# Kernel optimization log

Hardware: AMD Instinct MI355X
Metric: run time of the kernel (lower is better)

The kernel has to match this reference:

```python
import jax, jax.numpy as jnp
import numpy as np

GROUPS = 32
EPS = 1e-6


def group_norm(x, gamma, beta):
    b, c, h, w = x.shape
    xg = x.reshape(b, GROUPS, c // GROUPS, h, w)
    mu = xg.mean(axis=(2, 3, 4), keepdims=True)
    var = xg.var(axis=(2, 3, 4), keepdims=True)
    xn = ((xg - mu) * jax.lax.rsqrt(var + EPS)).reshape(b, c, h, w)
    return xn * gamma[None, :, None, None] + beta[None, :, None, None]


def conv1x1(x, w, b):
    # x: (b,c_in,h,w), w: (c_out,c_in), b: (c_out,)
    return jnp.einsum('oc,bchw->bohw', w, x) + b[None, :, None, None]


def setup_inputs() -> dict:
    key = jax.random.key(0)
    ks = jax.random.split(key, 10)
    c = 512
    scale = 1.0 / np.sqrt(c)
    inp = jax.random.normal(ks[0], (16, c, 32, 32), dtype=jnp.float32)
    return {
        'inp': inp,
        'gamma': jnp.ones((c,), jnp.float32),
        'beta': jnp.zeros((c,), jnp.float32),
        'Wq': jax.random.normal(ks[1], (c, c), jnp.float32) * scale,
        'bq': jnp.zeros((c,), jnp.float32),
        'Wk': jax.random.normal(ks[2], (c, c), jnp.float32) * scale,
        'bk': jnp.zeros((c,), jnp.float32),
        'Wv': jax.random.normal(ks[3], (c, c), jnp.float32) * scale,
        'bv': jnp.zeros((c,), jnp.float32),
        'Wo': jax.random.normal(ks[4], (c, c), jnp.float32) * scale,
        'bo': jnp.zeros((c,), jnp.float32),
    }


def reference(inp, gamma, beta, Wq, bq, Wk, bk, Wv, bv, Wo, bo):
    b, c, h, w = inp.shape
    x = group_norm(inp, gamma, beta)
    Q = conv1x1(x, Wq, bq).reshape(b, c, h * w)  # (b,c,n)
    K = conv1x1(x, Wk, bk).reshape(b, c, h * w)  # (b,c,m)
    V = conv1x1(x, Wv, bv).reshape(b, c, h * w)  # (b,c,m)
    # attn[b,n,m] = sum_c Q[b,c,n] * K[b,c,m], scaled then softmax over m
    attn = jnp.einsum('bcn,bcm->bnm', Q, K) / jnp.sqrt(jnp.float32(c))
    attn = jax.nn.softmax(attn, axis=2)
    # A[b,c,n] = sum_m V[b,c,m] * attn[b,n,m]  (== bmm(V, attn^T))
    A = jnp.einsum('bcm,bnm->bcn', V, attn).reshape(b, c, h, w)
    A = conv1x1(A, Wo, bo)
    return inp + A
```

## Files before the change

### kernel.cpp

```cpp
#include <hip/hip_runtime.h>

typedef unsigned short UST;
typedef __attribute__((ext_vector_type(8))) short bf16x8;
typedef __attribute__((ext_vector_type(8))) unsigned short us8;
typedef __attribute__((ext_vector_type(4))) float f32x4;

__device__ __forceinline__ UST f2bf(float f) {
  union { float f; unsigned int u; } x; x.f = f;
  unsigned int r = x.u + 0x7fffu + ((x.u >> 16) & 1u);
  return (UST)(r >> 16);
}
__device__ __forceinline__ float bf2f(UST h) {
  union { unsigned int u; float f; } x; x.u = ((unsigned int)h) << 16;
  return x.f;
}

__device__ __forceinline__ void sync_lds() {
  asm volatile("s_waitcnt lgkmcnt(0)\n\ts_barrier" ::: "memory");
}
__device__ __forceinline__ void barrier_nowait() {
  asm volatile("s_barrier" ::: "memory");
}

__global__ __launch_bounds__(256) void conv_w(
    const float4* __restrict__ wq, const float4* __restrict__ wk,
    const float4* __restrict__ wv, const float4* __restrict__ wo,
    ushort4* __restrict__ oqkv, ushort4* __restrict__ owo,
    const float4* __restrict__ bq4, const float4* __restrict__ bk4,
    const float4* __restrict__ bv4, float4* __restrict__ bqkv4) {
  int i = blockIdx.x * 256 + threadIdx.x;
  float4 v;
  v = wq[i]; oqkv[i]          = make_ushort4(f2bf(v.x), f2bf(v.y), f2bf(v.z), f2bf(v.w));
  v = wk[i]; oqkv[i + 65536]  = make_ushort4(f2bf(v.x), f2bf(v.y), f2bf(v.z), f2bf(v.w));
  v = wv[i]; oqkv[i + 131072] = make_ushort4(f2bf(v.x), f2bf(v.y), f2bf(v.z), f2bf(v.w));
  v = wo[i]; owo[i]           = make_ushort4(f2bf(v.x), f2bf(v.y), f2bf(v.z), f2bf(v.w));
  if (blockIdx.x < 2) {
    int t = blockIdx.x * 256 + threadIdx.x;
    if (t < 384) bqkv4[t] = (t < 128) ? bq4[t] : (t < 256 ? bk4[t - 128] : bv4[t - 256]);
  }
}

__global__ __launch_bounds__(256) void gn_fused(
    const float* __restrict__ inp, const float* __restrict__ gamma,
    const float* __restrict__ beta, UST* __restrict__ Xnt) {
  const int g = blockIdx.x & 31, b = blockIdx.x >> 5;
  const int tid = threadIdx.x;
  const float* base = inp + ((size_t)b * 32 + g) * 16384;
  const float4* p4 = (const float4*)base;
  float s = 0.f, ss = 0.f;
#pragma unroll
  for (int i = 0; i < 16; i++) {
    float4 t = p4[tid + i * 256];
    s += t.x + t.y + t.z + t.w;
    ss += t.x * t.x + t.y * t.y + t.z * t.z + t.w * t.w;
  }
  for (int o = 32; o >= 1; o >>= 1) { s += __shfl_xor(s, o); ss += __shfl_xor(ss, o); }
  __shared__ float red[8];
  __shared__ float mu_s, rstd_s;
  const int w = tid >> 6;
  if ((tid & 63) == 0) { red[w * 2] = s; red[w * 2 + 1] = ss; }
  __syncthreads();
  if (tid == 0) {
    float S1 = red[0] + red[2] + red[4] + red[6];
    float S2 = red[1] + red[3] + red[5] + red[7];
    float mu = S1 * (1.f / 16384.f);
    float var = S2 * (1.f / 16384.f) - mu * mu;
    mu_s = mu; rstd_s = rsqrtf(var + 1e-6f);
  }
  __syncthreads();
  const float mu = mu_s, rstd = rstd_s;
#pragma unroll
  for (int cc = 0; cc < 2; cc++) {
    const int ccg = g * 2 + cc;
    float sc[8], sh[8];
#pragma unroll
    for (int j = 0; j < 8; j++) {
      int ch = ccg * 8 + j;
      sc[j] = gamma[ch] * rstd;
      sh[j] = beta[ch] - mu * sc[j];
    }
#pragma unroll
    for (int i = 0; i < 4; i++) {
      const int n = tid + i * 256;
      us8 v;
#pragma unroll
      for (int j = 0; j < 8; j++) {
        float x = inp[((size_t)b * 512 + ccg * 8 + j) * 1024 + n];
        v[j] = f2bf(x * sc[j] + sh[j]);
      }
      *(us8*)(Xnt + (size_t)b * 524288 + (size_t)ccg * 8192 + (size_t)n * 8) = v;
    }
  }
}

__global__ __launch_bounds__(256) void softmax_k(const UST* __restrict__ S,
                                                 UST* __restrict__ P) {
  const int w = threadIdx.x >> 6, lane = threadIdx.x & 63;
  const size_t row = (size_t)blockIdx.x * 4 + w;
  const us8* Sr = (const us8*)(S + row * 1024);
  us8 a = Sr[lane], b = Sr[64 + lane];
  float v[16];
#pragma unroll
  for (int j = 0; j < 8; j++) { v[j] = bf2f(a[j]); v[8 + j] = bf2f(b[j]); }
  float m = v[0];
#pragma unroll
  for (int i = 1; i < 16; i++) m = fmaxf(m, v[i]);
#pragma unroll
  for (int o = 32; o >= 1; o >>= 1) m = fmaxf(m, __shfl_xor(m, o));
  float s = 0.f;
#pragma unroll
  for (int i = 0; i < 16; i++) { v[i] = __expf(v[i] - m); s += v[i]; }
#pragma unroll
  for (int o = 32; o >= 1; o >>= 1) s += __shfl_xor(s, o);
  const float rs = 1.f / s;
  us8* Pr = (us8*)(P + row * 1024);
  us8 oa, ob;
#pragma unroll
  for (int j = 0; j < 8; j++) { oa[j] = f2bf(v[j] * rs); ob[j] = f2bf(v[8 + j] * rs); }
  Pr[lane] = oa; Pr[64 + lane] = ob;
}

template <int EPI>
__global__ __launch_bounds__(256, 2) void gemm_bt(
    const UST* __restrict__ A, const UST* __restrict__ B, void* __restrict__ C,
    const float* __restrict__ bias, const float* __restrict__ extra, float scale,
    int K, int ldc,
    int rsA, int csA, int ssA, int rsB, int csB, int ssB,
    long zA, long zB, long zC) {
  __shared__ __align__(16) UST buf[10240];
  UST* lA = buf;
  UST* lB = buf + 5120;

  const int tid = threadIdx.x;
  const int z = blockIdx.z;
  const int m0 = blockIdx.y * 128;
  const int n0 = blockIdx.x * 128;
  const UST* Ab = A + (long)z * zA;
  const UST* Bb = B + (long)z * zB;

  const int w = tid >> 6, lane = tid & 63;
  const int quad = lane >> 4, l16 = lane & 15;
  const int wm = w >> 1, wn = w & 1;

  f32x4 acc[4][4];
#pragma unroll
  for (int i = 0; i < 4; i++)
#pragma unroll
    for (int j = 0; j < 4; j++) acc[i][j] = f32x4{0.f, 0.f, 0.f, 0.f};

  const int rowa = tid >> 2;
  const int kchunk = tid & 3;
  const UST* gA = Ab + (size_t)(m0 + rowa) * rsA + (size_t)kchunk * csA;
  const UST* gB = Bb + (size_t)(n0 + rowa) * rsB + (size_t)kchunk * csB;
  const size_t a64 = (size_t)64 * rsA, b64 = (size_t)64 * rsB;
  UST* wA = lA + rowa * 40 + kchunk * 8;
  UST* wB = lB + rowa * 40 + kchunk * 8;

  us8 pa0 = *(const us8*)gA, pa1 = *(const us8*)(gA + a64);
  us8 pb0 = *(const us8*)gB, pb1 = *(const us8*)(gB + b64);

  const int nk = K >> 5;
  for (int k = 0; k < nk; ++k) {
    us8 na0, na1, nb0, nb1;
    if (k + 1 < nk) {
      gA += ssA; gB += ssB;
      na0 = *(const us8*)gA; na1 = *(const us8*)(gA + a64);
      nb0 = *(const us8*)gB; nb1 = *(const us8*)(gB + b64);
    }
    if (k) barrier_nowait();
    *(us8*)wA = pa0; *(us8*)(wA + 2560) = pa1;
    *(us8*)wB = pb0; *(us8*)(wB + 2560) = pb1;
    sync_lds();
    bf16x8 af[4], bfr[4];
#pragma unroll
    for (int i = 0; i < 4; i++)
      af[i] = *(const bf16x8*)(lA + (wm * 64 + i * 16 + l16) * 40 + quad * 8);
#pragma unroll
    for (int j = 0; j < 4; j++)
      bfr[j] = *(const bf16x8*)(lB + (wn * 64 + j * 16 + l16) * 40 + quad * 8);
#pragma unroll
    for (int i = 0; i < 4; i++)
#pragma unroll
      for (int j = 0; j < 4; j++)
        acc[i][j] = __builtin_amdgcn_mfma_f32_16x16x32_bf16(af[i], bfr[j], acc[i][j], 0, 0, 0);
    pa0 = na0; pa1 = na1; pb0 = nb0; pb1 = nb1;
  }

  barrier_nowait();

  if constexpr (EPI == 4) {
    float* fbuf = (float*)buf;
    float* Cb = (float*)C + (long)z * zC;
    const float* Eb = extra + (long)z * zC;
#pragma unroll
    for (int p = 0; p < 4; ++p) {
      if (p) barrier_nowait();
      if (wm == (p >> 1)) {
#pragma unroll
        for (int ii = 0; ii < 2; ii++) {
          const int i = (p & 1) * 2 + ii;
#pragma unroll
          for (int j = 0; j < 4; j++)
#pragma unroll
            for (int r = 0; r < 4; r++)
              fbuf[(ii * 16 + quad * 4 + r) * 132 + wn * 64 + j * 16 + l16] = acc[i][j][r];
        }
      }
      sync_lds();
#pragma unroll
      for (int it = 0; it < 4; ++it) {
        int q = tid + it * 256;
        int row = q >> 5, colc = q & 31;
        int gr = m0 + p * 32 + row;
        size_t off = (size_t)gr * ldc + n0 + colc * 4;
        float4 v = *(float4*)&fbuf[row * 132 + colc * 4];
        float4 e = *(const float4*)&Eb[off];
        float bb = bias[gr];
        v.x += bb + e.x; v.y += bb + e.y; v.z += bb + e.z; v.w += bb + e.w;
        *(float4*)&Cb[off] = v;
      }
    }
  } else {
    const bool vreg = (EPI == 6) && (n0 >= 1024);
    if (!vreg) {
      UST* Cb = (UST*)C + (long)z * zC;
#pragma unroll
      for (int h = 0; h < 2; ++h) {
        if (h) barrier_nowait();
        if (wm == h) {
#pragma unroll
          for (int i = 0; i < 4; i++)
#pragma unroll
            for (int j = 0; j < 4; j++) {
              float bc = 0.f;
              if constexpr (EPI == 6) bc = bias[n0 + wn * 64 + j * 16 + l16];
#pragma unroll
              for (int r = 0; r < 4; r++) {
                float v = acc[i][j][r] + bc;
                if constexpr (EPI == 5) v *= scale;
                buf[(i * 16 + quad * 4 + r) * 136 + wn * 64 + j * 16 + l16] = f2bf(v);
              }
            }
        }
        sync_lds();
#pragma unroll
        for (int it = 0; it < 4; ++it) {
          int q = tid + it * 256;
          int row = q >> 4, colc = q & 15;
          us8 v = *(us8*)&buf[row * 136 + colc * 8];
          *(us8*)&Cb[(size_t)(m0 + h * 64 + row) * ldc + n0 + colc * 8] = v;
        }
      }
    } else {
      UST* Vb = (UST*)extra + (long)z * 524288;
#pragma unroll
      for (int h = 0; h < 2; ++h) {
        if (h) barrier_nowait();
        if (wn == h) {
#pragma unroll
          for (int i = 0; i < 4; i++)
#pragma unroll
            for (int j = 0; j < 4; j++) {
              const float bc = bias[n0 + wn * 64 + j * 16 + l16];
#pragma unroll
              for (int r = 0; r < 4; r++) {
                float v = acc[i][j][r] + bc;
                buf[(j * 16 + l16) * 136 + wm * 64 + i * 16 + quad * 4 + r] = f2bf(v);
              }
            }
        }
        sync_lds();
#pragma unroll
        for (int it = 0; it < 4; ++it) {
          int q = tid + it * 256;
          int c = q >> 4, mc = q & 15;
          us8 v = *(us8*)&buf[c * 136 + mc * 8];
          *(us8*)&Vb[(size_t)(n0 - 1024 + h * 64 + c) * 1024 + m0 + mc * 8] = v;
        }
      }
    }
  }
}

extern "C" void kernel_launch(void* const* d_in, const int* in_sizes, int n_in,
                              void* d_out, int out_size, void* d_ws, size_t ws_size,
                              hipStream_t stream) {
  const float* inp   = (const float*)d_in[0];
  const float* gamma = (const float*)d_in[1];
  const float* beta  = (const float*)d_in[2];
  const float* Wq    = (const float*)d_in[3];
  const float* bq    = (const float*)d_in[4];
  const float* Wk    = (const float*)d_in[5];
  const float* bk    = (const float*)d_in[6];
  const float* Wv    = (const float*)d_in[7];
  const float* bv    = (const float*)d_in[8];
  const float* Wo    = (const float*)d_in[9];
  const float* bo    = (const float*)d_in[10];
  float* out = (float*)d_out;
  char* ws = (char*)d_ws;

  UST*   Xnt   = (UST*)(ws);
  UST*   QKt   = (UST*)(ws + ((size_t)16 << 20));
  UST*   V     = (UST*)(ws + ((size_t)48 << 20));
  UST*   S     = (UST*)(ws + ((size_t)64 << 20));
  float* bqkv  = (float*)(ws + ((size_t)96 << 20));
  UST*   Wqkvb = (UST*)(ws + ((size_t)96 << 20) + 8192);
  UST*   Wob   = Wqkvb + 786432;
  UST*   P     = QKt;
  UST*   At    = Xnt;

  conv_w<<<256, 256, 0, stream>>>(
      (const float4*)Wq, (const float4*)Wk, (const float4*)Wv, (const float4*)Wo,
      (ushort4*)Wqkvb, (ushort4*)Wob,
      (const float4*)bq, (const float4*)bk, (const float4*)bv, (float4*)bqkv);
  gn_fused<<<512, 256, 0, stream>>>(inp, gamma, beta, Xnt);

  gemm_bt<6><<<dim3(12, 8, 16), 256, 0, stream>>>(
      Xnt, Wqkvb, QKt, bqkv, (const float*)V, 1.f,
      512, 1024, 8, 8192, 32768, 512, 8, 32, 524288, 0, 1048576);
  gemm_bt<5><<<dim3(8, 8, 16), 256, 0, stream>>>(
      QKt, QKt + 512, S, nullptr, nullptr, 0.04419417382415922f,
      512, 1024, 1024, 8, 32, 1024, 8, 32, 1048576, 1048576, 1048576);
  softmax_k<<<4096, 256, 0, stream>>>(S, P);
  gemm_bt<3><<<dim3(4, 8, 16), 256, 0, stream>>>(
      P, V, At, nullptr, nullptr, 1.f,
      1024, 512, 1024, 8, 32, 1024, 8, 32, 1048576, 524288, 524288);
  gemm_bt<4><<<dim3(8, 4, 16), 256, 0, stream>>>(
      Wob, At, out, bo, inp, 1.f,
      512, 1024, 512, 8, 32, 512, 8, 32, 0, 524288, 524288);
}
```

Before: 238.5 us.

## Double-buffer GEMM LDS tiles, merge prep kernels, swizzle QKV block order

```diff
diff --git a/kernel.cpp b/kernel.cpp
--- a/kernel.cpp
+++ b/kernel.cpp
@@ -22,29 +22,30 @@
   asm volatile("s_barrier" ::: "memory");
 }
 
-__global__ __launch_bounds__(256) void conv_w(
+__global__ __launch_bounds__(256) void prep(
+    const float* __restrict__ inp, const float* __restrict__ gamma,
+    const float* __restrict__ beta, UST* __restrict__ Xnt,
     const float4* __restrict__ wq, const float4* __restrict__ wk,
     const float4* __restrict__ wv, const float4* __restrict__ wo,
     ushort4* __restrict__ oqkv, ushort4* __restrict__ owo,
     const float4* __restrict__ bq4, const float4* __restrict__ bk4,
     const float4* __restrict__ bv4, float4* __restrict__ bqkv4) {
-  int i = blockIdx.x * 256 + threadIdx.x;
-  float4 v;
-  v = wq[i]; oqkv[i]          = make_ushort4(f2bf(v.x), f2bf(v.y), f2bf(v.z), f2bf(v.w));
-  v = wk[i]; oqkv[i + 65536]  = make_ushort4(f2bf(v.x), f2bf(v.y), f2bf(v.z), f2bf(v.w));
-  v = wv[i]; oqkv[i + 131072] = make_ushort4(f2bf(v.x), f2bf(v.y), f2bf(v.z), f2bf(v.w));
-  v = wo[i]; owo[i]           = make_ushort4(f2bf(v.x), f2bf(v.y), f2bf(v.z), f2bf(v.w));
-  if (blockIdx.x < 2) {
-    int t = blockIdx.x * 256 + threadIdx.x;
-    if (t < 384) bqkv4[t] = (t < 128) ? bq4[t] : (t < 256 ? bk4[t - 128] : bv4[t - 256]);
-  }
-}
-
-__global__ __launch_bounds__(256) void gn_fused(
-    const float* __restrict__ inp, const float* __restrict__ gamma,
-    const float* __restrict__ beta, UST* __restrict__ Xnt) {
+  const int tid = threadIdx.x;
+  if (blockIdx.x >= 512) {
+    const int wb = blockIdx.x - 512;
+    int i = wb * 256 + tid;
+    float4 v;
+    v = wq[i]; oqkv[i]          = make_ushort4(f2bf(v.x), f2bf(v.y), f2bf(v.z), f2bf(v.w));
+    v = wk[i]; oqkv[i + 65536]  = make_ushort4(f2bf(v.x), f2bf(v.y), f2bf(v.z), f2bf(v.w));
+    v = wv[i]; oqkv[i + 131072] = make_ushort4(f2bf(v.x), f2bf(v.y), f2bf(v.z), f2bf(v.w));
+    v = wo[i]; owo[i]           = make_ushort4(f2bf(v.x), f2bf(v.y), f2bf(v.z), f2bf(v.w));
+    if (wb < 2) {
+      int t = wb * 256 + tid;
+      if (t < 384) bqkv4[t] = (t < 128) ? bq4[t] : (t < 256 ? bk4[t - 128] : bv4[t - 256]);
+    }
+    return;
+  }
   const int g = blockIdx.x & 31, b = blockIdx.x >> 5;
-  const int tid = threadIdx.x;
   const float* base = inp + ((size_t)b * 32 + g) * 16384;
   const float4* p4 = (const float4*)base;
   float s = 0.f, ss = 0.f;
@@ -120,21 +121,30 @@
   Pr[lane] = oa; Pr[64 + lane] = ob;
 }
 
-template <int EPI>
+template <int EPI, bool SWZ>
 __global__ __launch_bounds__(256, 2) void gemm_bt(
     const UST* __restrict__ A, const UST* __restrict__ B, void* __restrict__ C,
     const float* __restrict__ bias, const float* __restrict__ extra, float scale,
     int K, int ldc,
     int rsA, int csA, int ssA, int rsB, int csB, int ssB,
     long zA, long zB, long zC) {
-  __shared__ __align__(16) UST buf[10240];
-  UST* lA = buf;
-  UST* lB = buf + 5120;
+  __shared__ __align__(16) UST buf[20480];
+  UST* l0A = buf;
+  UST* l0B = buf + 5120;
+  UST* l1A = buf + 10240;
+  UST* l1B = buf + 15360;
 
   const int tid = threadIdx.x;
-  const int z = blockIdx.z;
-  const int m0 = blockIdx.y * 128;
-  const int n0 = blockIdx.x * 128;
+  int m0, n0, z;
+  if constexpr (SWZ) {
+    int lin = blockIdx.x + 12 * (blockIdx.y + 8 * blockIdx.z);
+    int g = lin & 7, idx = lin >> 3;
+    int al = idx / 12, x = idx - al * 12;
+    int at = g * 16 + al;
+    m0 = (at & 7) * 128; n0 = x * 128; z = at >> 3;
+  } else {
+    m0 = blockIdx.y * 128; n0 = blockIdx.x * 128; z = blockIdx.z;
+  }
   const UST* Ab = A + (long)z * zA;
   const UST* Bb = B + (long)z * zB;
 
@@ -153,40 +163,51 @@
   const UST* gA = Ab + (size_t)(m0 + rowa) * rsA + (size_t)kchunk * csA;
   const UST* gB = Bb + (size_t)(n0 + rowa) * rsB + (size_t)kchunk * csB;
   const size_t a64 = (size_t)64 * rsA, b64 = (size_t)64 * rsB;
-  UST* wA = lA + rowa * 40 + kchunk * 8;
-  UST* wB = lB + rowa * 40 + kchunk * 8;
+  const int lw = rowa * 40 + kchunk * 8;
+
+  const int nk = K >> 5;
 
   us8 pa0 = *(const us8*)gA, pa1 = *(const us8*)(gA + a64);
   us8 pb0 = *(const us8*)gB, pb1 = *(const us8*)(gB + b64);
-
-  const int nk = K >> 5;
+  *(us8*)(l0A + lw) = pa0; *(us8*)(l0A + lw + 2560) = pa1;
+  *(us8*)(l0B + lw) = pb0; *(us8*)(l0B + lw + 2560) = pb1;
+  if (nk > 1) {
+    gA += ssA; gB += ssB;
+    pa0 = *(const us8*)gA; pa1 = *(const us8*)(gA + a64);
+    pb0 = *(const us8*)gB; pb1 = *(const us8*)(gB + b64);
+  }
+  sync_lds();
+
   for (int k = 0; k < nk; ++k) {
-    us8 na0, na1, nb0, nb1;
+    UST* curA = (k & 1) ? l1A : l0A;
+    UST* curB = (k & 1) ? l1B : l0B;
+    UST* nxtA = (k & 1) ? l0A : l1A;
+    UST* nxtB = (k & 1) ? l0B : l1B;
     if (k + 1 < nk) {
+      *(us8*)(nxtA + lw) = pa0; *(us8*)(nxtA + lw + 2560) = pa1;
+      *(us8*)(nxtB + lw) = pb0; *(us8*)(nxtB + lw + 2560) = pb1;
+    }
+    us8 qa0, qa1, qb0, qb1;
+    if (k + 2 < nk) {
       gA += ssA; gB += ssB;
-      na0 = *(const us8*)gA; na1 = *(const us8*)(gA + a64);
-      nb0 = *(const us8*)gB; nb1 = *(const us8*)(gB + b64);
-    }
-    if (k) barrier_nowait();
-    *(us8*)wA = pa0; *(us8*)(wA + 2560) = pa1;
-    *(us8*)wB = pb0; *(us8*)(wB + 2560) = pb1;
-    sync_lds();
+      qa0 = *(const us8*)gA; qa1 = *(const us8*)(gA + a64);
+      qb0 = *(const us8*)gB; qb1 = *(const us8*)(gB + b64);
+    }
     bf16x8 af[4], bfr[4];
 #pragma unroll
     for (int i = 0; i < 4; i++)
-      af[i] = *(const bf16x8*)(lA + (wm * 64 + i * 16 + l16) * 40 + quad * 8);
+      af[i] = *(const bf16x8*)(curA + (wm * 64 + i * 16 + l16) * 40 + quad * 8);
 #pragma unroll
     for (int j = 0; j < 4; j++)
-      bfr[j] = *(const bf16x8*)(lB + (wn * 64 + j * 16 + l16) * 40 + quad * 8);
+      bfr[j] = *(const bf16x8*)(curB + (wn * 64 + j * 16 + l16) * 40 + quad * 8);
 #pragma unroll
     for (int i = 0; i < 4; i++)
 #pragma unroll
       for (int j = 0; j < 4; j++)
         acc[i][j] = __builtin_amdgcn_mfma_f32_16x16x32_bf16(af[i], bfr[j], acc[i][j], 0, 0, 0);
-    pa0 = na0; pa1 = na1; pb0 = nb0; pb1 = nb1;
-  }
-
-  barrier_nowait();
+    sync_lds();
+    pa0 = qa0; pa1 = qa1; pb0 = qb0; pb1 = qb1;
+  }
 
   if constexpr (EPI == 4) {
     float* fbuf = (float*)buf;
@@ -309,23 +330,23 @@
   UST*   P     = QKt;
   UST*   At    = Xnt;
 
-  conv_w<<<256, 256, 0, stream>>>(
+  prep<<<768, 256, 0, stream>>>(
+      inp, gamma, beta, Xnt,
       (const float4*)Wq, (const float4*)Wk, (const float4*)Wv, (const float4*)Wo,
       (ushort4*)Wqkvb, (ushort4*)Wob,
       (const float4*)bq, (const float4*)bk, (const float4*)bv, (float4*)bqkv);
-  gn_fused<<<512, 256, 0, stream>>>(inp, gamma, beta, Xnt);
-
-  gemm_bt<6><<<dim3(12, 8, 16), 256, 0, stream>>>(
+
+  gemm_bt<6, true><<<dim3(12, 8, 16), 256, 0, stream>>>(
       Xnt, Wqkvb, QKt, bqkv, (const float*)V, 1.f,
       512, 1024, 8, 8192, 32768, 512, 8, 32, 524288, 0, 1048576);
-  gemm_bt<5><<<dim3(8, 8, 16), 256, 0, stream>>>(
+  gemm_bt<5, false><<<dim3(8, 8, 16), 256, 0, stream>>>(
       QKt, QKt + 512, S, nullptr, nullptr, 0.04419417382415922f,
       512, 1024, 1024, 8, 32, 1024, 8, 32, 1048576, 1048576, 1048576);
   softmax_k<<<4096, 256, 0, stream>>>(S, P);
-  gemm_bt<3><<<dim3(4, 8, 16), 256, 0, stream>>>(
+  gemm_bt<3, false><<<dim3(4, 8, 16), 256, 0, stream>>>(
       P, V, At, nullptr, nullptr, 1.f,
       1024, 512, 1024, 8, 32, 1024, 8, 32, 1048576, 524288, 524288);
-  gemm_bt<4><<<dim3(8, 4, 16), 256, 0, stream>>>(
+  gemm_bt<4, false><<<dim3(8, 4, 16), 256, 0, stream>>>(
       Wob, At, out, bo, inp, 1.f,
       512, 1024, 512, 8, 32, 512, 8, 32, 0, 524288, 524288);
 }
```

Result: no change. 240.5 us (+0.8%).
